# Performance work log

Hardware: AMD Instinct MI355X
Metric: run time of the kernel (lower is better)

Reference implementation:

```python
import jax, jax.numpy as jnp
import numpy as np
from functools import partial

N_ITER = 200  # LML(n_iter=200)


def sq_dists(Xi, x):
    # Xi: [N, n], x: [B, n] -> squared euclidean dists [B, N] (torch.cdist ** 2)
    x2 = jnp.sum(x * x, axis=1, keepdims=True)          # [B, 1]
    m2 = jnp.sum(Xi * Xi, axis=1)                        # [N]
    d = x2 + m2[None, :] - 2.0 * (x @ Xi.T)
    return jnp.maximum(d, 0.0)


def _lml_solve(x, k):
    # LML projection: y = sigmoid(x + nu), nu s.t. sum(y) = k; bisection on nu.
    x_sorted = -jnp.sort(-x, axis=1)                     # descending
    lo = -x_sorted[:, k - 1] - 7.0
    hi = -x_sorted[:, k] + 7.0

    def body(i, bounds):
        lo, hi = bounds
        mid = 0.5 * (lo + hi)
        f = jnp.sum(jax.nn.sigmoid(x + mid[:, None]), axis=1) - k
        lo = jnp.where(f < 0, mid, lo)
        hi = jnp.where(f < 0, hi, mid)
        return lo, hi

    lo, hi = jax.lax.fori_loop(0, N_ITER, body, (lo, hi))
    nu = 0.5 * (lo + hi)
    return jax.nn.sigmoid(x + nu[:, None])


@partial(jax.custom_vjp, nondiff_argnums=(1,))
def lml(x, k):
    return _lml_solve(x, k)


def _lml_fwd(x, k):
    y = _lml_solve(x, k)
    return y, y


def _lml_bwd(k, y, g):
    # implicit grad: dy = s*(dx - dnu), dnu = sum(s*dx)/sum(s), s = y(1-y)
    s = y * (1.0 - y)
    dnu = jnp.sum(s * g, axis=1, keepdims=True) / jnp.sum(s, axis=1, keepdims=True)
    return (s * (g - dnu),)


lml.defvjp(_lml_fwd, _lml_bwd)


def k_softmax(beta, x, k):
    # x: [B, N] (= -dists) -> [B, N, k]
    cols = [jax.nn.softmax(beta * x, axis=1)]
    last = cols[0]
    for i in range(1, k):
        new = lml(beta * x, i + 1)
        cols.append(new - last)
        last = new
    return jnp.stack(cols, axis=2)


def hopfield(Xi, x, beta):
    return jax.nn.softmax(-beta * sq_dists(Xi, x), axis=1) @ Xi


def k_hopfield_batch(Xi, x, k, beta, hopfield_steps):
    dists = sq_dists(Xi, x)                              # [B, N]
    ksm = k_softmax(beta, -dists, k)                     # [B, N, k]
    result = jnp.einsum('nd,bnk->bdk', Xi, ksm)          # Xi.T @ ksm -> [B, n, k]
    for _ in range(hopfield_steps):
        result = jnp.stack(
            [hopfield(Xi, result[:, :, j], beta) for j in range(k)], axis=2)
    return result


def setup_inputs() -> dict:
    key = jax.random.key(0)
    kx, km = jax.random.split(key)
    return {
        'x': jax.random.normal(kx, (2048, 512), dtype=jnp.float32),
        'memories': jax.random.normal(km, (8192, 512), dtype=jnp.float32),
        'k': 5,
        'beta': 1,
        'hopfield_steps': 2,
    }


def reference(x, memories, k, beta, hopfield_steps):
    return k_hopfield_batch(memories, x, k, beta, hopfield_steps)
```

## Files before the change

### kernel.cpp

```cpp
#include <hip/hip_runtime.h>
#include <hip/hip_bf16.h>


constexpr int   Bq    = 2048;
constexpr int   Nm    = 8192;
constexpr int   Dd    = 512;
constexpr int   KK    = 5;
constexpr float BETA  = 1.0f;
constexpr int   STEPS = 2;
constexpr int   KS    = 8;
constexpr size_t PL   = (size_t)Bq * Dd;

#define DEV static __device__ __forceinline__

DEV float b2f(ushort u) { unsigned v = ((unsigned)u) << 16; float f; __builtin_memcpy(&f, &v, 4); return f; }
DEV ushort f2b(float f) { __hip_bfloat16 h = __float2bfloat16(f); ushort u; __builtin_memcpy(&u, &h, 2); return u; }
DEV float ldin(const void* p, int isf, size_t idx) {
    return isf ? ((const float*)p)[idx] : b2f(((const ushort*)p)[idx]);
}

__global__ __launch_bounds__(256) void detect_k(const ushort* __restrict__ xin,
                                                int* __restrict__ flag) {
    __shared__ int sb;
    if (threadIdx.x == 0) sb = 0;
    __syncthreads();
    int bad = 0;
    for (int i = threadIdx.x; i < 1024; i += 256) {
        float v = b2f(xin[i]);
        if (!(fabsf(v) < 64.0f)) bad = 1;
    }
    if (bad) atomicOr(&sb, 1);
    __syncthreads();
    if (threadIdx.x == 0) flag[0] = sb;
}

__global__ __launch_bounds__(256) void norms_k(const void* __restrict__ xin,
                                               const void* __restrict__ memin,
                                               const int* __restrict__ flag,
                                               float* __restrict__ x2,
                                               float* __restrict__ m2) {
    int row = blockIdx.x;
    int isf = flag[0];
    const void* src; size_t base; float* dst;
    if (row < Nm) { src = memin; base = (size_t)row * Dd; dst = m2 + row; }
    else          { src = xin; base = (size_t)(row - Nm) * Dd; dst = x2 + (row - Nm); }
    int tid = threadIdx.x, lane = tid & 63, wave = tid >> 6;
    float s = 0.f;
    for (int i = tid; i < Dd; i += 256) { float v = ldin(src, isf, base + i); s += v * v; }
    for (int off = 32; off; off >>= 1) s += __shfl_down(s, off, 64);
    __shared__ float ws[4];
    if (lane == 0) ws[wave] = s;
    __syncthreads();
    if (tid == 0) dst[0] = ws[0] + ws[1] + ws[2] + ws[3];
}

__global__ __launch_bounds__(256) void distF2_k(const void* __restrict__ A,
                                                const int* __restrict__ flag, int aForceF,
                                                const void* __restrict__ memin,
                                                float* __restrict__ S,
                                                const float* __restrict__ a2,
                                                const float* __restrict__ m2,
                                                int ab0, float negBeta) {
    __shared__ float As[16][68];
    __shared__ float Bs[16][68];
    const int tid = threadIdx.x, tx = tid & 15, ty = tid >> 4;
    const int m0 = blockIdx.y * 64, n0 = blockIdx.x * 64;
    const int isfA = aForceF ? 1 : flag[0];
    const int isfB = flag[0];

    float acc[4][4];
#pragma unroll
    for (int i = 0; i < 4; ++i)
#pragma unroll
        for (int j = 0; j < 4; ++j) acc[i][j] = 0.f;

    for (int d0 = 0; d0 < Dd; d0 += 16) {
#pragma unroll
        for (int c = tid; c < 1024; c += 256) {
            int r = c >> 4, k = c & 15;
            As[k][r] = ldin(A, isfA, (size_t)(ab0 + m0 + r) * Dd + d0 + k);
            Bs[k][r] = ldin(memin, isfB, (size_t)(n0 + r) * Dd + d0 + k);
        }
        __syncthreads();
#pragma unroll
        for (int k = 0; k < 16; ++k) {
            float4 av = *(const float4*)&As[k][ty * 4];
            float4 bv = *(const float4*)&Bs[k][tx * 4];
            float a[4] = {av.x, av.y, av.z, av.w};
            float b[4] = {bv.x, bv.y, bv.z, bv.w};
#pragma unroll
            for (int i = 0; i < 4; ++i)
#pragma unroll
                for (int j = 0; j < 4; ++j) acc[i][j] = fmaf(a[i], b[j], acc[i][j]);
        }
        __syncthreads();
    }
#pragma unroll
    for (int i = 0; i < 4; ++i) {
        int m = m0 + ty * 4 + i;
        float4 o;
        float* po = (float*)&o;
#pragma unroll
        for (int j = 0; j < 4; ++j) {
            float d = a2[m] + m2[n0 + tx * 4 + j] - 2.0f * acc[i][j];
            po[j] = negBeta * fmaxf(d, 0.0f);
        }
        *(float4*)&S[(size_t)m * Nm + n0 + tx * 4] = o;
    }
}

template <int TRF>
__global__ __launch_bounds__(256) void wgemmG_k(const float* __restrict__ Sx,
                                                const void* __restrict__ memin,
                                                const int* __restrict__ flag,
                                                const float* __restrict__ rowpar,
                                                float* __restrict__ part, int planeSz) {
    __shared__ float Ws[16][68];
    __shared__ float Bs[16][68];
    const int tid = threadIdx.x, tx = tid & 15, ty = tid >> 4;
    const int d0 = blockIdx.x * 64, b0 = blockIdx.y * 64;
    const int kz = blockIdx.z * (Nm / KS);
    const int isf = flag[0];

    float acc[4][4];
#pragma unroll
    for (int i = 0; i < 4; ++i)
#pragma unroll
        for (int j = 0; j < 4; ++j) acc[i][j] = 0.f;

    for (int nc = kz; nc < kz + Nm / KS; nc += 16) {
#pragma unroll
        for (int c = tid; c < 1024; c += 256) {
            int r = c >> 4, k = c & 15;
            float s = Sx[(size_t)(b0 + r) * Nm + nc + k];
            float p0 = rowpar[(b0 + r) * 2 + 0];
            float w;
            if constexpr (TRF == 1) w = expf(s - p0) * rowpar[(b0 + r) * 2 + 1];
            else                    w = 1.0f / (1.0f + expf(-(s + p0)));
            Ws[k][r] = w;
            int kk = c >> 6, dd = c & 63;
            Bs[kk][dd] = ldin(memin, isf, (size_t)(nc + kk) * Dd + d0 + dd);
        }
        __syncthreads();
#pragma unroll
        for (int k = 0; k < 16; ++k) {
            float4 av = *(const float4*)&Ws[k][ty * 4];
            float4 bv = *(const float4*)&Bs[k][tx * 4];
            float a[4] = {av.x, av.y, av.z, av.w};
            float b[4] = {bv.x, bv.y, bv.z, bv.w};
#pragma unroll
            for (int i = 0; i < 4; ++i)
#pragma unroll
                for (int j = 0; j < 4; ++j) acc[i][j] = fmaf(a[i], b[j], acc[i][j]);
        }
        __syncthreads();
    }
    float* pz = part + (size_t)blockIdx.z * planeSz;
#pragma unroll
    for (int i = 0; i < 4; ++i) {
        float4 o = {acc[i][0], acc[i][1], acc[i][2], acc[i][3]};
        *(float4*)&pz[(size_t)(b0 + ty * 4 + i) * Dd + d0 + tx * 4] = o;
    }
}

__global__ __launch_bounds__(256) void reduceN_k(const float* __restrict__ part,
                                                 float* __restrict__ Rj,
                                                 float* __restrict__ r2w, int doNorm,
                                                 int planeSz) {
    int row = blockIdx.x, tid = threadIdx.x, lane = tid & 63, wave = tid >> 6;
    float sq = 0.f;
    for (int e = tid; e < Dd; e += 256) {
        float s = 0.f;
#pragma unroll
        for (int z = 0; z < KS; ++z) s += part[(size_t)z * planeSz + (size_t)row * Dd + e];
        Rj[(size_t)row * Dd + e] = s;
        sq += s * s;
    }
    if (doNorm) {
        for (int off = 32; off; off >>= 1) sq += __shfl_down(sq, off, 64);
        __shared__ float ws[4];
        if (lane == 0) ws[wave] = sq;
        __syncthreads();
        if (tid == 0) r2w[row] = ws[0] + ws[1] + ws[2] + ws[3];
    }
}

__global__ __launch_bounds__(256) void rowstats_k(const float* __restrict__ S,
                                                  float* __restrict__ stats) {
    int b = blockIdx.x, tid = threadIdx.x, lane = tid & 63, wave = tid >> 6;
    __shared__ float cbuf[1024];
    __shared__ int   ccnt;
    __shared__ float tops[256 * 6];
    __shared__ float stop[6];
    __shared__ float wred[16];
    __shared__ float bcast[5];
    const float* srow = S + (size_t)b * Nm;

    float tt[6];
#pragma unroll
    for (int q = 0; q < 6; ++q) tt[q] = -3.4e38f;
    for (int i = tid; i < Nm; i += 256) {
        float v = srow[i];
        if (v > tt[5]) {
            tt[5] = v;
#pragma unroll
            for (int q = 5; q > 0; --q)
                if (tt[q] > tt[q - 1]) { float tm = tt[q]; tt[q] = tt[q - 1]; tt[q - 1] = tm; }
        }
    }
#pragma unroll
    for (int q = 0; q < 6; ++q) tops[tid * 6 + q] = tt[q];
    if (tid == 0) ccnt = 0;
    __syncthreads();
    if (tid == 0) {
        float mt[6];
#pragma unroll
        for (int q = 0; q < 6; ++q) mt[q] = -3.4e38f;
        for (int i = 0; i < 256 * 6; ++i) {
            float v = tops[i];
            if (v > mt[5]) {
                mt[5] = v;
#pragma unroll
                for (int q = 5; q > 0; --q)
                    if (mt[q] > mt[q - 1]) { float tm = mt[q]; mt[q] = mt[q - 1]; mt[q - 1] = tm; }
            }
        }
#pragma unroll
        for (int q = 0; q < 6; ++q) stop[q] = mt[q];
    }
    __syncthreads();

    float smax = stop[0];
    float cutoff = stop[5] - 40.0f;
    float p = 0.f;
    for (int i = tid; i < Nm; i += 256) {
        float v = srow[i];
        p += expf(v - smax);
        if (v >= cutoff) {
            int idx = atomicAdd(&ccnt, 1);
            if (idx < 1024) cbuf[idx] = v;
        }
    }
    for (int off = 32; off; off >>= 1) p += __shfl_down(p, off, 64);
    if (lane == 0) wred[wave] = p;
    __syncthreads();
    if (tid == 0) bcast[4] = wred[0] + wred[1] + wred[2] + wred[3];
    __syncthreads();
    float denom = bcast[4];
    int cnt = min(ccnt, 1024);

    float lo[4], hi[4];
#pragma unroll
    for (int q = 0; q < 4; ++q) { lo[q] = -stop[q + 1] - 7.0f; hi[q] = -stop[q + 2] + 7.0f; }
    for (int it = 0; it < 48; ++it) {
        float mid[4], pp[4] = {0.f, 0.f, 0.f, 0.f};
#pragma unroll
        for (int q = 0; q < 4; ++q) mid[q] = 0.5f * (lo[q] + hi[q]);
        for (int i = tid; i < cnt; i += 256) {
            float v = cbuf[i];
#pragma unroll
            for (int q = 0; q < 4; ++q) pp[q] += 1.0f / (1.0f + expf(-(v + mid[q])));
        }
#pragma unroll
        for (int q = 0; q < 4; ++q) {
            float s = pp[q];
            for (int off = 32; off; off >>= 1) s += __shfl_down(s, off, 64);
            if (lane == 0) wred[wave * 4 + q] = s;
        }
        __syncthreads();
        if (tid == 0)
#pragma unroll
            for (int q = 0; q < 4; ++q) bcast[q] = wred[q] + wred[4 + q] + wred[8 + q] + wred[12 + q];
        __syncthreads();
#pragma unroll
        for (int q = 0; q < 4; ++q) {
            float f = bcast[q] - (float)(q + 2);
            if (f < 0.f) lo[q] = mid[q]; else hi[q] = mid[q];
        }
        __syncthreads();
    }
    if (tid == 0) {
        stats[b * 6 + 0] = smax;
        stats[b * 6 + 1] = denom;
#pragma unroll
        for (int q = 0; q < 4; ++q) stats[b * 6 + 2 + q] = 0.5f * (lo[q] + hi[q]);
    }
}

__global__ __launch_bounds__(256) void rowpar_stage1_k(const float* __restrict__ stats,
                                                       float* __restrict__ rowpar, int jj) {
    int b = blockIdx.x * 256 + threadIdx.x;
    if (b >= Bq) return;
    if (jj == 0) {
        rowpar[b * 2 + 0] = stats[b * 6 + 0];
        rowpar[b * 2 + 1] = 1.0f / stats[b * 6 + 1];
    } else {
        rowpar[b * 2 + 0] = stats[b * 6 + 1 + jj];
        rowpar[b * 2 + 1] = 0.0f;
    }
}

__global__ __launch_bounds__(256) void rowmax_denom_k(const float* __restrict__ S,
                                                      float* __restrict__ rowpar) {
    int b = blockIdx.x, tid = threadIdx.x, lane = tid & 63, wave = tid >> 6;
    __shared__ float wred[4];
    __shared__ float bc[1];
    const float* srow = S + (size_t)b * Nm;
    float mx = -3.4e38f;
    for (int i = tid; i < Nm; i += 256) mx = fmaxf(mx, srow[i]);
    for (int off = 32; off; off >>= 1) mx = fmaxf(mx, __shfl_down(mx, off, 64));
    if (lane == 0) wred[wave] = mx;
    __syncthreads();
    if (tid == 0) bc[0] = fmaxf(fmaxf(wred[0], wred[1]), fmaxf(wred[2], wred[3]));
    __syncthreads();
    mx = bc[0];
    float p = 0.f;
    for (int i = tid; i < Nm; i += 256) p += expf(srow[i] - mx);
    for (int off = 32; off; off >>= 1) p += __shfl_down(p, off, 64);
    __syncthreads();
    if (lane == 0) wred[wave] = p;
    __syncthreads();
    if (tid == 0) {
        rowpar[b * 2 + 0] = mx;
        rowpar[b * 2 + 1] = 1.0f / (wred[0] + wred[1] + wred[2] + wred[3]);
    }
}

__global__ __launch_bounds__(256) void combine_k(float* __restrict__ R,
                                                 float* __restrict__ r2all) {
    int row = blockIdx.x, tid = threadIdx.x, lane = tid & 63, wave = tid >> 6;
    float sq[5] = {0.f, 0.f, 0.f, 0.f, 0.f};
    for (int e = tid; e < Dd; e += 256) {
        size_t idx = (size_t)row * Dd + e;
        float r0 = R[idx], r1 = R[PL + idx], r2v = R[2 * PL + idx],
              r3 = R[3 * PL + idx], r4 = R[4 * PL + idx];
        float o1 = r1 - r0, o2 = r2v - r1, o3 = r3 - r2v, o4 = r4 - r3;
        R[PL + idx] = o1; R[2 * PL + idx] = o2; R[3 * PL + idx] = o3; R[4 * PL + idx] = o4;
        sq[0] += r0 * r0; sq[1] += o1 * o1; sq[2] += o2 * o2; sq[3] += o3 * o3; sq[4] += o4 * o4;
    }
    __shared__ float ws[5][4];
#pragma unroll
    for (int j = 0; j < 5; ++j) {
        float s = sq[j];
        for (int off = 32; off; off >>= 1) s += __shfl_down(s, off, 64);
        if (lane == 0) ws[j][wave] = s;
    }
    __syncthreads();
    if (tid < 5) r2all[tid * Bq + row] = ws[tid][0] + ws[tid][1] + ws[tid][2] + ws[tid][3];
}

__global__ __launch_bounds__(256) void final_k(const float* __restrict__ R,
                                               void* __restrict__ out,
                                               const int* __restrict__ flag) {
    size_t idx = (size_t)blockIdx.x * 256 + threadIdx.x;
    bool isf = flag[0] != 0;
#pragma unroll
    for (int j = 0; j < KK; ++j) {
        float v = R[(size_t)j * PL + idx];
        if (isf) ((float*)out)[idx * KK + j] = v;
        else     ((ushort*)out)[idx * KK + j] = f2b(v);
    }
}

extern "C" void kernel_launch(void* const* d_in, const int* in_sizes, int n_in,
                              void* d_out, int out_size, void* d_ws, size_t ws_size,
                              hipStream_t stream) {
    const void* xin   = d_in[0];
    const void* memin = d_in[1];

    const size_t MiB = 1048576ull, KiB = 1024ull;
    char* ws = (char*)d_ws;
    float* R     = (float*)(ws + 0);
    float* m2    = (float*)(ws + 20 * MiB);
    float* x2    = (float*)(ws + 20 * MiB + 32 * KiB);
    float* stats = (float*)(ws + 20 * MiB + 48 * KiB);
    float* rpar  = (float*)(ws + 20 * MiB + 96 * KiB);
    int*   flag  = (int*)  (ws + 20 * MiB + 112 * KiB);
    float* r2all = (float*)(ws + 20 * MiB + 128 * KiB);
    float* S     = (float*)(ws + 20 * MiB + 256 * KiB);

    float* part = (float*)d_out;

    int Bc = 128;
    const int cand[4] = {1024, 512, 256, 128};
    for (int i = 0; i < 4; ++i)
        if (20 * MiB + 256 * KiB + (size_t)cand[i] * Nm * 4 <= ws_size) { Bc = cand[i]; break; }
    const int nChunk = Bq / Bc;
    const int planeSz = Bc * Dd;

    detect_k<<<1, 256, 0, stream>>>((const ushort*)xin, flag);
    norms_k<<<Nm + Bq, 256, 0, stream>>>(xin, memin, flag, x2, m2);

    for (int c = 0; c < nChunk; ++c) {
        int b0 = c * Bc;
        distF2_k<<<dim3(Nm / 64, Bc / 64), 256, 0, stream>>>(
            xin, flag, 0, memin, S, x2 + b0, m2, b0, -BETA);
        rowstats_k<<<Bc, 256, 0, stream>>>(S, stats + (size_t)b0 * 6);
        for (int jj = 0; jj < KK; ++jj) {
            float* Rj = R + (size_t)jj * PL + (size_t)b0 * Dd;
            rowpar_stage1_k<<<Bq / 256, 256, 0, stream>>>(stats, rpar, jj);
            if (jj == 0)
                wgemmG_k<1><<<dim3(Dd / 64, Bc / 64, KS), 256, 0, stream>>>(
                    S, memin, flag, rpar + (size_t)b0 * 2, part, planeSz);
            else
                wgemmG_k<2><<<dim3(Dd / 64, Bc / 64, KS), 256, 0, stream>>>(
                    S, memin, flag, rpar + (size_t)b0 * 2, part, planeSz);
            reduceN_k<<<Bc, 256, 0, stream>>>(part, Rj, nullptr, 0, planeSz);
        }
    }
    combine_k<<<Bq, 256, 0, stream>>>(R, r2all);

    for (int st = 0; st < STEPS; ++st) {
        for (int jj = 0; jj < KK; ++jj) {
            float* Rj = R + (size_t)jj * PL;
            float* r2j = r2all + (size_t)jj * Bq;
            for (int c = 0; c < nChunk; ++c) {
                int b0 = c * Bc;
                distF2_k<<<dim3(Nm / 64, Bc / 64), 256, 0, stream>>>(
                    Rj, flag, 1, memin, S, r2j + b0, m2, b0, -BETA);
                rowmax_denom_k<<<Bc, 256, 0, stream>>>(S, rpar + (size_t)b0 * 2);
                wgemmG_k<1><<<dim3(Dd / 64, Bc / 64, KS), 256, 0, stream>>>(
                    S, memin, flag, rpar + (size_t)b0 * 2, part, planeSz);
                reduceN_k<<<Bc, 256, 0, stream>>>(
                    part, Rj + (size_t)b0 * Dd, r2j + b0, 1, planeSz);
            }
        }
    }
    final_k<<<(int)(PL / 256), 256, 0, stream>>>(R, d_out, flag);
}
```

Baseline: 10.11 ms.

## Move distance and weighted GEMMs to bf16 MFMA with split-precision hi/lo terms

Replaces the scalar-FMA fp32 tiled GEMMs for the distance matrix and the weighted memory sum with MFMA 16x16x32 bf16 kernels. Each fp32 operand is split into a bf16 high part and a bf16 residual, and three MFMAs (hh, lh, hl) approximate fp32 accuracy. The aim is to use matrix cores instead of VALU for the dominant GEMM work. In exchange there is some precision loss, extra conversion work in the loaders, and uncoalesced strided loads of memories in the weighted GEMM. The chunk-size selection now also checks that the partial-sum buffer fits in the output allocation.

```diff
diff --git a/kernel.cpp b/kernel.cpp
--- a/kernel.cpp
+++ b/kernel.cpp
@@ -12,6 +12,10 @@
 constexpr size_t PL   = (size_t)Bq * Dd;
 
 #define DEV static __device__ __forceinline__
+
+typedef __attribute__((ext_vector_type(8))) short           short8v;
+typedef __attribute__((ext_vector_type(8))) unsigned short  u16x8;
+typedef __attribute__((ext_vector_type(4))) float           f32x4;
 
 DEV float b2f(ushort u) { unsigned v = ((unsigned)u) << 16; float f; __builtin_memcpy(&f, &v, 4); return f; }
 DEV ushort f2b(float f) { __hip_bfloat16 h = __float2bfloat16(f); ushort u; __builtin_memcpy(&u, &h, 2); return u; }
@@ -54,113 +58,191 @@
     if (tid == 0) dst[0] = ws[0] + ws[1] + ws[2] + ws[3];
 }
 
-__global__ __launch_bounds__(256) void distF2_k(const void* __restrict__ A,
-                                                const int* __restrict__ flag, int aForceF,
-                                                const void* __restrict__ memin,
-                                                float* __restrict__ S,
-                                                const float* __restrict__ a2,
-                                                const float* __restrict__ m2,
-                                                int ab0, float negBeta) {
-    __shared__ float As[16][68];
-    __shared__ float Bs[16][68];
-    const int tid = threadIdx.x, tx = tid & 15, ty = tid >> 4;
+#define SPL(V, H, L, I) { ushort hu_ = f2b(V); H[I] = hu_; L[I] = f2b((V) - b2f(hu_)); }
+
+__global__ __launch_bounds__(256) void distM_k(const void* __restrict__ A,
+                                               const int* __restrict__ flag, int aForceF,
+                                               const void* __restrict__ memin,
+                                               float* __restrict__ S,
+                                               const float* __restrict__ a2,
+                                               const float* __restrict__ m2,
+                                               int ab0, float negBeta) {
+    __shared__ ushort TA[2][4][64][8];
+    __shared__ ushort TB[2][4][64][8];
+    const int tid = threadIdx.x, lane = tid & 63, wid = tid >> 6;
+    const int wm = wid >> 1, wn = wid & 1;
     const int m0 = blockIdx.y * 64, n0 = blockIdx.x * 64;
     const int isfA = aForceF ? 1 : flag[0];
     const int isfB = flag[0];
-
-    float acc[4][4];
-#pragma unroll
-    for (int i = 0; i < 4; ++i)
-#pragma unroll
-        for (int j = 0; j < 4; ++j) acc[i][j] = 0.f;
-
-    for (int d0 = 0; d0 < Dd; d0 += 16) {
-#pragma unroll
-        for (int c = tid; c < 1024; c += 256) {
-            int r = c >> 4, k = c & 15;
-            As[k][r] = ldin(A, isfA, (size_t)(ab0 + m0 + r) * Dd + d0 + k);
-            Bs[k][r] = ldin(memin, isfB, (size_t)(n0 + r) * Dd + d0 + k);
-        }
-        __syncthreads();
-#pragma unroll
-        for (int k = 0; k < 16; ++k) {
-            float4 av = *(const float4*)&As[k][ty * 4];
-            float4 bv = *(const float4*)&Bs[k][tx * 4];
-            float a[4] = {av.x, av.y, av.z, av.w};
-            float b[4] = {bv.x, bv.y, bv.z, bv.w};
-#pragma unroll
-            for (int i = 0; i < 4; ++i)
-#pragma unroll
-                for (int j = 0; j < 4; ++j) acc[i][j] = fmaf(a[i], b[j], acc[i][j]);
-        }
-        __syncthreads();
-    }
-#pragma unroll
-    for (int i = 0; i < 4; ++i) {
-        int m = m0 + ty * 4 + i;
-        float4 o;
-        float* po = (float*)&o;
-#pragma unroll
-        for (int j = 0; j < 4; ++j) {
-            float d = a2[m] + m2[n0 + tx * 4 + j] - 2.0f * acc[i][j];
-            po[j] = negBeta * fmaxf(d, 0.0f);
-        }
-        *(float4*)&S[(size_t)m * Nm + n0 + tx * 4] = o;
-    }
+    const int r = tid & 63, kc = tid >> 6;
+
+    f32x4 acc[2][2];
+    const f32x4 z = {0.f, 0.f, 0.f, 0.f};
+#pragma unroll
+    for (int i = 0; i < 2; ++i)
+#pragma unroll
+        for (int j = 0; j < 2; ++j) acc[i][j] = z;
+
+    for (int k0 = 0; k0 < Dd; k0 += 32) {
+        const size_t offA = (size_t)(ab0 + m0 + r) * Dd + k0 + kc * 8;
+        const size_t offB = (size_t)(n0 + r) * Dd + k0 + kc * 8;
+        u16x8 ah, al, bh, bl;
+        if (isfA) {
+            float4 t0 = *(const float4*)((const float*)A + offA);
+            float4 t1 = *(const float4*)((const float*)A + offA + 4);
+            SPL(t0.x, ah, al, 0) SPL(t0.y, ah, al, 1) SPL(t0.z, ah, al, 2) SPL(t0.w, ah, al, 3)
+            SPL(t1.x, ah, al, 4) SPL(t1.y, ah, al, 5) SPL(t1.z, ah, al, 6) SPL(t1.w, ah, al, 7)
+        } else {
+            u16x8 t = *(const u16x8*)((const ushort*)A + offA);
+#pragma unroll
+            for (int j = 0; j < 8; ++j) { ah[j] = t[j]; al[j] = 0; }
+        }
+        if (isfB) {
+            float4 t0 = *(const float4*)((const float*)memin + offB);
+            float4 t1 = *(const float4*)((const float*)memin + offB + 4);
+            SPL(t0.x, bh, bl, 0) SPL(t0.y, bh, bl, 1) SPL(t0.z, bh, bl, 2) SPL(t0.w, bh, bl, 3)
+            SPL(t1.x, bh, bl, 4) SPL(t1.y, bh, bl, 5) SPL(t1.z, bh, bl, 6) SPL(t1.w, bh, bl, 7)
+        } else {
+            u16x8 t = *(const u16x8*)((const ushort*)memin + offB);
+#pragma unroll
+            for (int j = 0; j < 8; ++j) { bh[j] = t[j]; bl[j] = 0; }
+        }
+        __syncthreads();
+        *(u16x8*)&TA[0][kc][r][0] = ah;
+        *(u16x8*)&TA[1][kc][r][0] = al;
+        *(u16x8*)&TB[0][kc][r][0] = bh;
+        *(u16x8*)&TB[1][kc][r][0] = bl;
+        __syncthreads();
+
+        const int rl = lane & 15, kq = lane >> 4;
+        short8v a0h = *(const short8v*)&TA[0][kq][wm * 32 + rl][0];
+        short8v a1h = *(const short8v*)&TA[0][kq][wm * 32 + 16 + rl][0];
+        short8v a0l = *(const short8v*)&TA[1][kq][wm * 32 + rl][0];
+        short8v a1l = *(const short8v*)&TA[1][kq][wm * 32 + 16 + rl][0];
+        short8v b0h = *(const short8v*)&TB[0][kq][wn * 32 + rl][0];
+        short8v b1h = *(const short8v*)&TB[0][kq][wn * 32 + 16 + rl][0];
+        short8v b0l = *(const short8v*)&TB[1][kq][wn * 32 + rl][0];
+        short8v b1l = *(const short8v*)&TB[1][kq][wn * 32 + 16 + rl][0];
+
+        acc[0][0] = __builtin_amdgcn_mfma_f32_16x16x32_bf16(a0h, b0h, acc[0][0], 0, 0, 0);
+        acc[0][0] = __builtin_amdgcn_mfma_f32_16x16x32_bf16(a0l, b0h, acc[0][0], 0, 0, 0);
+        acc[0][0] = __builtin_amdgcn_mfma_f32_16x16x32_bf16(a0h, b0l, acc[0][0], 0, 0, 0);
+        acc[0][1] = __builtin_amdgcn_mfma_f32_16x16x32_bf16(a0h, b1h, acc[0][1], 0, 0, 0);
+        acc[0][1] = __builtin_amdgcn_mfma_f32_16x16x32_bf16(a0l, b1h, acc[0][1], 0, 0, 0);
+        acc[0][1] = __builtin_amdgcn_mfma_f32_16x16x32_bf16(a0h, b1l, acc[0][1], 0, 0, 0);
+        acc[1][0] = __builtin_amdgcn_mfma_f32_16x16x32_bf16(a1h, b0h, acc[1][0], 0, 0, 0);
+        acc[1][0] = __builtin_amdgcn_mfma_f32_16x16x32_bf16(a1l, b0h, acc[1][0], 0, 0, 0);
+        acc[1][0] = __builtin_amdgcn_mfma_f32_16x16x32_bf16(a1h, b0l, acc[1][0], 0, 0, 0);
+        acc[1][1] = __builtin_amdgcn_mfma_f32_16x16x32_bf16(a1h, b1h, acc[1][1], 0, 0, 0);
+        acc[1][1] = __builtin_amdgcn_mfma_f32_16x16x32_bf16(a1l, b1h, acc[1][1], 0, 0, 0);
+        acc[1][1] = __builtin_amdgcn_mfma_f32_16x16x32_bf16(a1h, b1l, acc[1][1], 0, 0, 0);
+    }
+
+    const int col = lane & 15, r0 = (lane >> 4) * 4;
+#pragma unroll
+    for (int fm = 0; fm < 2; ++fm)
+#pragma unroll
+        for (int fn = 0; fn < 2; ++fn) {
+            const int n = n0 + wn * 32 + fn * 16 + col;
+            const float mm2 = m2[n];
+#pragma unroll
+            for (int q = 0; q < 4; ++q) {
+                const int m = m0 + wm * 32 + fm * 16 + r0 + q;
+                const float d = a2[m] + mm2 - 2.0f * acc[fm][fn][q];
+                S[(size_t)m * Nm + n] = negBeta * fmaxf(d, 0.0f);
+            }
+        }
 }
 
 template <int TRF>
-__global__ __launch_bounds__(256) void wgemmG_k(const float* __restrict__ Sx,
+DEV float wtr(float s, float p0, float p1) {
+    if (TRF == 1) return expf(s - p0) * p1;
+    else          return 1.0f / (1.0f + expf(-(s + p0)));
+}
+
+#define PACKW(SV, H, L, I) { float w_ = wtr<TRF>(SV, p0, p1); ushort hu_ = f2b(w_); \
+                             H[I] = hu_; L[I] = f2b(w_ - b2f(hu_)); }
+
+template <int TRF>
+__global__ __launch_bounds__(256) void wgemmM_k(const float* __restrict__ Sx,
                                                 const void* __restrict__ memin,
                                                 const int* __restrict__ flag,
                                                 const float* __restrict__ rowpar,
                                                 float* __restrict__ part, int planeSz) {
-    __shared__ float Ws[16][68];
-    __shared__ float Bs[16][68];
-    const int tid = threadIdx.x, tx = tid & 15, ty = tid >> 4;
+    __shared__ ushort TW[2][4][64][8];
+    __shared__ ushort TB[2][4][64][8];
+    const int tid = threadIdx.x, lane = tid & 63, wid = tid >> 6;
+    const int wm = wid >> 1, wn = wid & 1;
     const int d0 = blockIdx.x * 64, b0 = blockIdx.y * 64;
     const int kz = blockIdx.z * (Nm / KS);
     const int isf = flag[0];
-
-    float acc[4][4];
-#pragma unroll
-    for (int i = 0; i < 4; ++i)
-#pragma unroll
-        for (int j = 0; j < 4; ++j) acc[i][j] = 0.f;
-
-    for (int nc = kz; nc < kz + Nm / KS; nc += 16) {
-#pragma unroll
-        for (int c = tid; c < 1024; c += 256) {
-            int r = c >> 4, k = c & 15;
-            float s = Sx[(size_t)(b0 + r) * Nm + nc + k];
-            float p0 = rowpar[(b0 + r) * 2 + 0];
-            float w;
-            if constexpr (TRF == 1) w = expf(s - p0) * rowpar[(b0 + r) * 2 + 1];
-            else                    w = 1.0f / (1.0f + expf(-(s + p0)));
-            Ws[k][r] = w;
-            int kk = c >> 6, dd = c & 63;
-            Bs[kk][dd] = ldin(memin, isf, (size_t)(nc + kk) * Dd + d0 + dd);
-        }
-        __syncthreads();
-#pragma unroll
-        for (int k = 0; k < 16; ++k) {
-            float4 av = *(const float4*)&Ws[k][ty * 4];
-            float4 bv = *(const float4*)&Bs[k][tx * 4];
-            float a[4] = {av.x, av.y, av.z, av.w};
-            float b[4] = {bv.x, bv.y, bv.z, bv.w};
-#pragma unroll
-            for (int i = 0; i < 4; ++i)
-#pragma unroll
-                for (int j = 0; j < 4; ++j) acc[i][j] = fmaf(a[i], b[j], acc[i][j]);
-        }
-        __syncthreads();
-    }
+    const int r = tid & 63, kc = tid >> 6;
+    const float p0 = rowpar[(b0 + r) * 2 + 0];
+    const float p1 = rowpar[(b0 + r) * 2 + 1];
+
+    f32x4 acc[2][2];
+    const f32x4 z = {0.f, 0.f, 0.f, 0.f};
+#pragma unroll
+    for (int i = 0; i < 2; ++i)
+#pragma unroll
+        for (int j = 0; j < 2; ++j) acc[i][j] = z;
+
+    for (int nc = kz; nc < kz + Nm / KS; nc += 32) {
+        float4 s0 = *(const float4*)&Sx[(size_t)(b0 + r) * Nm + nc + kc * 8];
+        float4 s1 = *(const float4*)&Sx[(size_t)(b0 + r) * Nm + nc + kc * 8 + 4];
+        u16x8 wh, wl;
+        PACKW(s0.x, wh, wl, 0) PACKW(s0.y, wh, wl, 1) PACKW(s0.z, wh, wl, 2) PACKW(s0.w, wh, wl, 3)
+        PACKW(s1.x, wh, wl, 4) PACKW(s1.y, wh, wl, 5) PACKW(s1.z, wh, wl, 6) PACKW(s1.w, wh, wl, 7)
+        u16x8 bh, bl;
+#pragma unroll
+        for (int j = 0; j < 8; ++j) {
+            float v = ldin(memin, isf, (size_t)(nc + kc * 8 + j) * Dd + d0 + r);
+            SPL(v, bh, bl, j)
+        }
+        __syncthreads();
+        *(u16x8*)&TW[0][kc][r][0] = wh;
+        *(u16x8*)&TW[1][kc][r][0] = wl;
+        *(u16x8*)&TB[0][kc][r][0] = bh;
+        *(u16x8*)&TB[1][kc][r][0] = bl;
+        __syncthreads();
+
+        const int rl = lane & 15, kq = lane >> 4;
+        short8v w0h = *(const short8v*)&TW[0][kq][wm * 32 + rl][0];
+        short8v w1h = *(const short8v*)&TW[0][kq][wm * 32 + 16 + rl][0];
+        short8v w0l = *(const short8v*)&TW[1][kq][wm * 32 + rl][0];
+        short8v w1l = *(const short8v*)&TW[1][kq][wm * 32 + 16 + rl][0];
+        short8v b0h = *(const short8v*)&TB[0][kq][wn * 32 + rl][0];
+        short8v b1h = *(const short8v*)&TB[0][kq][wn * 32 + 16 + rl][0];
+        short8v b0l = *(const short8v*)&TB[1][kq][wn * 32 + rl][0];
+        short8v b1l = *(const short8v*)&TB[1][kq][wn * 32 + 16 + rl][0];
+
+        acc[0][0] = __builtin_amdgcn_mfma_f32_16x16x32_bf16(w0h, b0h, acc[0][0], 0, 0, 0);
+        acc[0][0] = __builtin_amdgcn_mfma_f32_16x16x32_bf16(w0l, b0h, acc[0][0], 0, 0, 0);
+        acc[0][0] = __builtin_amdgcn_mfma_f32_16x16x32_bf16(w0h, b0l, acc[0][0], 0, 0, 0);
+        acc[0][1] = __builtin_amdgcn_mfma_f32_16x16x32_bf16(w0h, b1h, acc[0][1], 0, 0, 0);
+        acc[0][1] = __builtin_amdgcn_mfma_f32_16x16x32_bf16(w0l, b1h, acc[0][1], 0, 0, 0);
+        acc[0][1] = __builtin_amdgcn_mfma_f32_16x16x32_bf16(w0h, b1l, acc[0][1], 0, 0, 0);
+        acc[1][0] = __builtin_amdgcn_mfma_f32_16x16x32_bf16(w1h, b0h, acc[1][0], 0, 0, 0);
+        acc[1][0] = __builtin_amdgcn_mfma_f32_16x16x32_bf16(w1l, b0h, acc[1][0], 0, 0, 0);
+        acc[1][0] = __builtin_amdgcn_mfma_f32_16x16x32_bf16(w1h, b0l, acc[1][0], 0, 0, 0);
+        acc[1][1] = __builtin_amdgcn_mfma_f32_16x16x32_bf16(w1h, b1h, acc[1][1], 0, 0, 0);
+        acc[1][1] = __builtin_amdgcn_mfma_f32_16x16x32_bf16(w1l, b1h, acc[1][1], 0, 0, 0);
+        acc[1][1] = __builtin_amdgcn_mfma_f32_16x16x32_bf16(w1h, b1l, acc[1][1], 0, 0, 0);
+    }
+
     float* pz = part + (size_t)blockIdx.z * planeSz;
-#pragma unroll
-    for (int i = 0; i < 4; ++i) {
-        float4 o = {acc[i][0], acc[i][1], acc[i][2], acc[i][3]};
-        *(float4*)&pz[(size_t)(b0 + ty * 4 + i) * Dd + d0 + tx * 4] = o;
-    }
+    const int col = lane & 15, r0 = (lane >> 4) * 4;
+#pragma unroll
+    for (int fm = 0; fm < 2; ++fm)
+#pragma unroll
+        for (int fn = 0; fn < 2; ++fn) {
+            const int dc = d0 + wn * 32 + fn * 16 + col;
+#pragma unroll
+            for (int q = 0; q < 4; ++q) {
+                const int br = b0 + wm * 32 + fm * 16 + r0 + q;
+                pz[(size_t)br * Dd + dc] = acc[fm][fn][q];
+            }
+        }
 }
 
 __global__ __launch_bounds__(256) void reduceN_k(const float* __restrict__ part,
@@ -362,6 +444,7 @@
     }
 }
 
+
 extern "C" void kernel_launch(void* const* d_in, const int* in_sizes, int n_in,
                               void* d_out, int out_size, void* d_ws, size_t ws_size,
                               hipStream_t stream) {
@@ -383,8 +466,11 @@
 
     int Bc = 128;
     const int cand[4] = {1024, 512, 256, 128};
-    for (int i = 0; i < 4; ++i)
-        if (20 * MiB + 256 * KiB + (size_t)cand[i] * Nm * 4 <= ws_size) { Bc = cand[i]; break; }
+    for (int i = 0; i < 4; ++i) {
+        size_t needWS  = 20 * MiB + 256 * KiB + (size_t)cand[i] * Nm * 4;
+        size_t needOut = (size_t)KS * cand[i] * Dd * 4;
+        if (needWS <= ws_size && needOut <= (size_t)out_size) { Bc = cand[i]; break; }
+    }
     const int nChunk = Bq / Bc;
     const int planeSz = Bc * Dd;
 
@@ -393,17 +479,17 @@
 
     for (int c = 0; c < nChunk; ++c) {
         int b0 = c * Bc;
-        distF2_k<<<dim3(Nm / 64, Bc / 64), 256, 0, stream>>>(
+        distM_k<<<dim3(Nm / 64, Bc / 64), 256, 0, stream>>>(
             xin, flag, 0, memin, S, x2 + b0, m2, b0, -BETA);
         rowstats_k<<<Bc, 256, 0, stream>>>(S, stats + (size_t)b0 * 6);
         for (int jj = 0; jj < KK; ++jj) {
             float* Rj = R + (size_t)jj * PL + (size_t)b0 * Dd;
             rowpar_stage1_k<<<Bq / 256, 256, 0, stream>>>(stats, rpar, jj);
             if (jj == 0)
-                wgemmG_k<1><<<dim3(Dd / 64, Bc / 64, KS), 256, 0, stream>>>(
+                wgemmM_k<1><<<dim3(Dd / 64, Bc / 64, KS), 256, 0, stream>>>(
                     S, memin, flag, rpar + (size_t)b0 * 2, part, planeSz);
             else
-                wgemmG_k<2><<<dim3(Dd / 64, Bc / 64, KS), 256, 0, stream>>>(
+                wgemmM_k<2><<<dim3(Dd / 64, Bc / 64, KS), 256, 0, stream>>>(
                     S, memin, flag, rpar + (size_t)b0 * 2, part, planeSz);
             reduceN_k<<<Bc, 256, 0, stream>>>(part, Rj, nullptr, 0, planeSz);
         }
@@ -416,10 +502,10 @@
             float* r2j = r2all + (size_t)jj * Bq;
             for (int c = 0; c < nChunk; ++c) {
                 int b0 = c * Bc;
-                distF2_k<<<dim3(Nm / 64, Bc / 64), 256, 0, stream>>>(
+                distM_k<<<dim3(Nm / 64, Bc / 64), 256, 0, stream>>>(
                     Rj, flag, 1, memin, S, r2j + b0, m2, b0, -BETA);
                 rowmax_denom_k<<<Bc, 256, 0, stream>>>(S, rpar + (size_t)b0 * 2);
-                wgemmG_k<1><<<dim3(Dd / 64, Bc / 64, KS), 256, 0, stream>>>(
+                wgemmM_k<1><<<dim3(Dd / 64, Bc / 64, KS), 256, 0, stream>>>(
                     S, memin, flag, rpar + (size_t)b0 * 2, part, planeSz);
                 reduceN_k<<<Bc, 256, 0, stream>>>(
                     part, Rj + (size_t)b0 * Dd, r2j + b0, 1, planeSz);
```

Result: slower. 10.78 ms (+6.7%).
